# Performance work log

Measured on AMD Instinct MI355X. Metric: run time of the kernel, lower is better.

The kernel has to match this reference:

```python
import jax, jax.numpy as jnp
import numpy as np

EPS = 1e-5

def layer_norm(x, g, b):
    m = jnp.mean(x, axis=-1, keepdims=True)
    v = jnp.var(x, axis=-1, keepdims=True)
    return (x - m) * jax.lax.rsqrt(v + EPS) * g + b

def setup_inputs() -> dict:
    key = jax.random.key(0)
    ks = jax.random.split(key, 10)
    A, T, c_s, c_z, c_atom, c_pair = 1024, 256, 384, 128, 128, 16
    tok = jax.random.randint(ks[0], (A,), 0, T)
    a2t = jax.nn.one_hot(tok, T, dtype=jnp.float32)  # [A, T] one-hot atom->token map
    return {
        "atom_to_token_index": a2t,
        "cl": jax.random.normal(ks[1], (A, c_atom), jnp.float32),
        "plm": jax.random.normal(ks[2], (A, A, c_pair), jnp.float32),
        "ql": jax.random.normal(ks[3], (A, c_atom), jnp.float32),
        "s_trunk": jax.random.normal(ks[4], (T, c_s), jnp.float32),
        "zij": jax.random.normal(ks[5], (T, T, c_z), jnp.float32),
        "rl": jax.random.normal(ks[6], (A, 3), jnp.float32),
        "ln_s_g": jnp.ones((c_s,), jnp.float32),
        "ln_s_b": jnp.zeros((c_s,), jnp.float32),
        "W_s": jax.random.normal(ks[7], (c_s, c_atom), jnp.float32) / np.sqrt(c_s),
        "ln_z_g": jnp.ones((c_z,), jnp.float32),
        "ln_z_b": jnp.zeros((c_z,), jnp.float32),
        "W_z": jax.random.normal(ks[8], (c_z, c_pair), jnp.float32) / np.sqrt(c_z),
        "W_r": jax.random.normal(ks[9], (3, c_atom), jnp.float32) / np.sqrt(3.0),
    }

def reference(atom_to_token_index, cl, plm, ql, s_trunk, zij, rl,
              ln_s_g, ln_s_b, W_s, ln_z_g, ln_z_b, W_z, W_r):
    a2t = atom_to_token_index  # [A, T]
    # token -> atom gather of single rep: sum_t a2t[a,t] * s_trunk[t,:]  -> [A, c_s]
    s_atom = jnp.einsum('at,tc->ac', a2t, s_trunk)
    cl = cl + layer_norm(s_atom, ln_s_g, ln_s_b) @ W_s  # [A, c_atom]
    # token-pair -> atom-pair gather: sum_{t,u} a2t[a,t] a2t[b,u] zij[t,u,:]
    # factored into two one-hot contractions (same math as the dense one-hot outer product)
    z_half = jnp.einsum('at,tuz->auz', a2t, zij)      # [A, T, c_z]
    z_atom = jnp.einsum('auz,bu->abz', z_half, a2t)    # [A, A, c_z]
    plm = plm + layer_norm(z_atom, ln_z_g, ln_z_b) @ W_z  # [A, A, c_pair]
    ql = ql + rl @ W_r  # [A, c_atom]
    return (cl, plm, ql)
```

## Files before the change

kernel.cpp:

```cpp
#include <hip/hip_runtime.h>

#define A_N 1024
#define T_N 256
#define CS 384
#define CZ 128
#define CA 128
#define CP 16
#define LN_EPS 1e-5f

#define ZROWS 64
#define ZPAD 132

__global__ __launch_bounds__(128) void atom_kernel(
        const float* __restrict__ a2t,
        const float* __restrict__ cl,
        const float* __restrict__ ql,
        const float* __restrict__ s_trunk,
        const float* __restrict__ rl,
        const float* __restrict__ g,
        const float* __restrict__ b,
        const float* __restrict__ W_s,
        const float* __restrict__ W_r,
        int* __restrict__ tok,
        float* __restrict__ out_cl,
        float* __restrict__ out_ql) {
    int a = blockIdx.x, tid = threadIdx.x;
    __shared__ int ta_sh;
    __shared__ float xs[CS];
    __shared__ float2 wred[2];

    float v0 = a2t[a * T_N + tid];
    float v1 = a2t[a * T_N + 128 + tid];
    if (v0 > 0.5f) ta_sh = tid;
    if (v1 > 0.5f) ta_sh = 128 + tid;
    __syncthreads();
    int ta = ta_sh;
    if (tid == 0) tok[a] = ta;

    float sum = 0.f, sq = 0.f;
    #pragma unroll
    for (int j = 0; j < 3; ++j) {
        float v = s_trunk[ta * CS + j * 128 + tid];
        xs[j * 128 + tid] = v;
        sum += v; sq += v * v;
    }
    #pragma unroll
    for (int off = 32; off > 0; off >>= 1) {
        sum += __shfl_down(sum, off);
        sq  += __shfl_down(sq,  off);
    }
    if ((tid & 63) == 0) wred[tid >> 6] = make_float2(sum, sq);
    __syncthreads();
    float s  = wred[0].x + wred[1].x;
    float ss = wred[0].y + wred[1].y;
    float m = s * (1.f / CS);
    float rstd = rsqrtf(ss * (1.f / CS) - m * m + LN_EPS);

    float acc = 0.f;
    for (int k = 0; k < CS; ++k) {
        float zn = (xs[k] - m) * rstd * g[k] + b[k];
        acc = fmaf(zn, W_s[k * CA + tid], acc);
    }
    out_cl[a * CA + tid] = cl[a * CA + tid] + acc;

    float r0 = rl[a * 3 + 0], r1 = rl[a * 3 + 1], r2 = rl[a * 3 + 2];
    out_ql[a * CA + tid] = ql[a * CA + tid]
                         + r0 * W_r[tid] + r1 * W_r[CA + tid] + r2 * W_r[2 * CA + tid];
}

__global__ __launch_bounds__(256) void z_kernel(
        const float* __restrict__ zij,
        const float* __restrict__ g,
        const float* __restrict__ b,
        const float* __restrict__ W_z,
        float* __restrict__ Yz) {
    __shared__ float xs[ZROWS * ZPAD];
    __shared__ float wgt[CP * ZPAD];
    __shared__ float2 parts[ZROWS][4];
    __shared__ float msh[ZROWS], rsh[ZROWS];
    __shared__ float2 gb_part[16][16];
    __shared__ float Gw_sh[CP], Bw_sh[CP];

    int t = threadIdx.x;
    size_t base = (size_t)blockIdx.x * ZROWS * CZ;

    const float4* zv = (const float4*)(zij + base);
    #pragma unroll
    for (int n = 0; n < 8; ++n) {
        int idx = n * 256 + t;
        int r = idx >> 5, c = idx & 31;
        *(float4*)&xs[r * ZPAD + c * 4] = zv[idx];
    }
    {
        int j = t & 15, seg = t >> 4;
        float sg = 0.f, sb = 0.f;
        #pragma unroll
        for (int i = 0; i < 8; ++i) {
            int k = seg * 8 + i;
            float w = W_z[k * CP + j];
            float gw = g[k] * w;
            wgt[j * ZPAD + k] = gw;
            sg += gw;
            sb = fmaf(b[k], w, sb);
        }
        gb_part[seg][j] = make_float2(sg, sb);
    }
    __syncthreads();
    if (t < CP) {
        float sg = 0.f, sb = 0.f;
        #pragma unroll
        for (int s = 0; s < 16; ++s) { float2 p = gb_part[s][t]; sg += p.x; sb += p.y; }
        Gw_sh[t] = sg; Bw_sh[t] = sb;
    }
    {
        int r = t >> 2, q = t & 3;
        const float* row = &xs[r * ZPAD + q * 32];
        float s = 0.f, ss = 0.f;
        #pragma unroll
        for (int i = 0; i < 8; ++i) {
            float4 v = *(const float4*)&row[i * 4];
            s += v.x + v.y + v.z + v.w;
            ss += v.x * v.x + v.y * v.y + v.z * v.z + v.w * v.w;
        }
        parts[r][q] = make_float2(s, ss);
    }
    __syncthreads();
    if (t < ZROWS) {
        float s = 0.f, ss = 0.f;
        #pragma unroll
        for (int q = 0; q < 4; ++q) { float2 p = parts[t][q]; s += p.x; ss += p.y; }
        float m = s * (1.f / CZ);
        msh[t] = m;
        rsh[t] = rsqrtf(ss * (1.f / CZ) - m * m + LN_EPS);
    }
    __syncthreads();

    int j = t & 15, rg = t >> 4;
    float acc[4] = {0.f, 0.f, 0.f, 0.f};
    const float* wrow = &wgt[j * ZPAD];
    #pragma unroll 4
    for (int k4 = 0; k4 < 32; ++k4) {
        float4 w = *(const float4*)&wrow[k4 * 4];
        #pragma unroll
        for (int rr = 0; rr < 4; ++rr) {
            float4 x = *(const float4*)&xs[(rg * 4 + rr) * ZPAD + k4 * 4];
            acc[rr] = fmaf(x.x, w.x, acc[rr]);
            acc[rr] = fmaf(x.y, w.y, acc[rr]);
            acc[rr] = fmaf(x.z, w.z, acc[rr]);
            acc[rr] = fmaf(x.w, w.w, acc[rr]);
        }
    }
    float gwj = Gw_sh[j], bwj = Bw_sh[j];
    #pragma unroll
    for (int rr = 0; rr < 4; ++rr) {
        int r = rg * 4 + rr;
        float y = rsh[r] * (acc[rr] - msh[r] * gwj) + bwj;
        size_t grow = (size_t)blockIdx.x * ZROWS + r;
        Yz[grow * CP + j] = y;
    }
}

__global__ __launch_bounds__(256) void plm_kernel(
        const float* __restrict__ plm,
        const float* __restrict__ Yz,
        const int* __restrict__ tok,
        float* __restrict__ out) {
    int tid = threadIdx.x;
    size_t i = (size_t)blockIdx.x * 256 + tid;
    int ta = tok[blockIdx.x >> 4];
    int bb = ((blockIdx.x & 15) << 6) + (tid >> 2);
    int tb = tok[bb];
    float4 pv = ((const float4*)plm)[i];
    float4 yv = ((const float4*)(Yz + (size_t)(ta * T_N + tb) * CP))[tid & 3];
    float4 o;
    o.x = pv.x + yv.x; o.y = pv.y + yv.y;
    o.z = pv.z + yv.z; o.w = pv.w + yv.w;
    ((float4*)out)[i] = o;
}

extern "C" void kernel_launch(void* const* d_in, const int* in_sizes, int n_in,
                              void* d_out, int out_size, void* d_ws, size_t ws_size,
                              hipStream_t stream) {
    const float* a2t     = (const float*)d_in[0];
    const float* cl      = (const float*)d_in[1];
    const float* plm     = (const float*)d_in[2];
    const float* ql      = (const float*)d_in[3];
    const float* s_trunk = (const float*)d_in[4];
    const float* zij     = (const float*)d_in[5];
    const float* rl      = (const float*)d_in[6];
    const float* ln_s_g  = (const float*)d_in[7];
    const float* ln_s_b  = (const float*)d_in[8];
    const float* W_s     = (const float*)d_in[9];
    const float* ln_z_g  = (const float*)d_in[10];
    const float* ln_z_b  = (const float*)d_in[11];
    const float* W_z     = (const float*)d_in[12];
    const float* W_r     = (const float*)d_in[13];

    int*   tok = (int*)d_ws;
    float* Yz  = (float*)((char*)d_ws + 4096);

    float* out_cl  = (float*)d_out;
    float* out_plm = out_cl + A_N * CA;
    float* out_ql  = out_plm + (size_t)A_N * A_N * CP;

    atom_kernel<<<A_N, 128, 0, stream>>>(a2t, cl, ql, s_trunk, rl,
                                         ln_s_g, ln_s_b, W_s, W_r,
                                         tok, out_cl, out_ql);
    z_kernel<<<(T_N * T_N) / ZROWS, 256, 0, stream>>>(zij, ln_z_g, ln_z_b, W_z, Yz);
    plm_kernel<<<((size_t)A_N * A_N * CP / 4) / 256, 256, 0, stream>>>(plm, Yz, tok, out_plm);
}
```

Measured before the change: 200.9 us.

## Use bf16 MFMA for z projection and compute s projection per token

Measured after the change: 191.9 us. 4.5% less time.

```diff
diff --git a/kernel.cpp b/kernel.cpp
--- a/kernel.cpp
+++ b/kernel.cpp
@@ -8,39 +8,22 @@
 #define CP 16
 #define LN_EPS 1e-5f
 
-#define ZROWS 64
-#define ZPAD 132
-
-__global__ __launch_bounds__(128) void atom_kernel(
-        const float* __restrict__ a2t,
-        const float* __restrict__ cl,
-        const float* __restrict__ ql,
+typedef __bf16  bf16x8 __attribute__((ext_vector_type(8)));
+typedef float   f32x4  __attribute__((ext_vector_type(4)));
+
+__global__ __launch_bounds__(128) void s_kernel(
         const float* __restrict__ s_trunk,
-        const float* __restrict__ rl,
         const float* __restrict__ g,
         const float* __restrict__ b,
         const float* __restrict__ W_s,
-        const float* __restrict__ W_r,
-        int* __restrict__ tok,
-        float* __restrict__ out_cl,
-        float* __restrict__ out_ql) {
-    int a = blockIdx.x, tid = threadIdx.x;
-    __shared__ int ta_sh;
+        float* __restrict__ Ys) {
+    int t = blockIdx.x, tid = threadIdx.x;
     __shared__ float xs[CS];
     __shared__ float2 wred[2];
-
-    float v0 = a2t[a * T_N + tid];
-    float v1 = a2t[a * T_N + 128 + tid];
-    if (v0 > 0.5f) ta_sh = tid;
-    if (v1 > 0.5f) ta_sh = 128 + tid;
-    __syncthreads();
-    int ta = ta_sh;
-    if (tid == 0) tok[a] = ta;
-
     float sum = 0.f, sq = 0.f;
     #pragma unroll
     for (int j = 0; j < 3; ++j) {
-        float v = s_trunk[ta * CS + j * 128 + tid];
+        float v = s_trunk[t * CS + j * 128 + tid];
         xs[j * 128 + tid] = v;
         sum += v; sq += v * v;
     }
@@ -56,41 +39,34 @@
     float m = s * (1.f / CS);
     float rstd = rsqrtf(ss * (1.f / CS) - m * m + LN_EPS);
 
-    float acc = 0.f;
-    for (int k = 0; k < CS; ++k) {
-        float zn = (xs[k] - m) * rstd * g[k] + b[k];
-        acc = fmaf(zn, W_s[k * CA + tid], acc);
-    }
-    out_cl[a * CA + tid] = cl[a * CA + tid] + acc;
-
-    float r0 = rl[a * 3 + 0], r1 = rl[a * 3 + 1], r2 = rl[a * 3 + 2];
-    out_ql[a * CA + tid] = ql[a * CA + tid]
-                         + r0 * W_r[tid] + r1 * W_r[CA + tid] + r2 * W_r[2 * CA + tid];
-}
-
-__global__ __launch_bounds__(256) void z_kernel(
+    float a0 = 0.f, a1 = 0.f, a2 = 0.f, a3 = 0.f;
+    for (int k = 0; k < CS; k += 4) {
+        float z0 = (xs[k + 0] - m) * rstd * g[k + 0] + b[k + 0];
+        float z1 = (xs[k + 1] - m) * rstd * g[k + 1] + b[k + 1];
+        float z2 = (xs[k + 2] - m) * rstd * g[k + 2] + b[k + 2];
+        float z3 = (xs[k + 3] - m) * rstd * g[k + 3] + b[k + 3];
+        a0 = fmaf(z0, W_s[(k + 0) * CA + tid], a0);
+        a1 = fmaf(z1, W_s[(k + 1) * CA + tid], a1);
+        a2 = fmaf(z2, W_s[(k + 2) * CA + tid], a2);
+        a3 = fmaf(z3, W_s[(k + 3) * CA + tid], a3);
+    }
+    Ys[t * CA + tid] = (a0 + a1) + (a2 + a3);
+}
+
+#define WSTRIDE 136
+
+__global__ __launch_bounds__(256) void z_mfma_kernel(
         const float* __restrict__ zij,
         const float* __restrict__ g,
         const float* __restrict__ b,
         const float* __restrict__ W_z,
         float* __restrict__ Yz) {
-    __shared__ float xs[ZROWS * ZPAD];
-    __shared__ float wgt[CP * ZPAD];
-    __shared__ float2 parts[ZROWS][4];
-    __shared__ float msh[ZROWS], rsh[ZROWS];
+    __shared__ __bf16 wb[CP * WSTRIDE];
     __shared__ float2 gb_part[16][16];
     __shared__ float Gw_sh[CP], Bw_sh[CP];
 
     int t = threadIdx.x;
-    size_t base = (size_t)blockIdx.x * ZROWS * CZ;
-
-    const float4* zv = (const float4*)(zij + base);
-    #pragma unroll
-    for (int n = 0; n < 8; ++n) {
-        int idx = n * 256 + t;
-        int r = idx >> 5, c = idx & 31;
-        *(float4*)&xs[r * ZPAD + c * 4] = zv[idx];
-    }
+
     {
         int j = t & 15, seg = t >> 4;
         float sg = 0.f, sb = 0.f;
@@ -99,7 +75,7 @@
             int k = seg * 8 + i;
             float w = W_z[k * CP + j];
             float gw = g[k] * w;
-            wgt[j * ZPAD + k] = gw;
+            wb[j * WSTRIDE + k] = (__bf16)gw;
             sg += gw;
             sb = fmaf(b[k], w, sb);
         }
@@ -112,52 +88,83 @@
         for (int s = 0; s < 16; ++s) { float2 p = gb_part[s][t]; sg += p.x; sb += p.y; }
         Gw_sh[t] = sg; Bw_sh[t] = sb;
     }
-    {
-        int r = t >> 2, q = t & 3;
-        const float* row = &xs[r * ZPAD + q * 32];
-        float s = 0.f, ss = 0.f;
-        #pragma unroll
-        for (int i = 0; i < 8; ++i) {
-            float4 v = *(const float4*)&row[i * 4];
-            s += v.x + v.y + v.z + v.w;
-            ss += v.x * v.x + v.y * v.y + v.z * v.z + v.w * v.w;
-        }
-        parts[r][q] = make_float2(s, ss);
-    }
-    __syncthreads();
-    if (t < ZROWS) {
-        float s = 0.f, ss = 0.f;
-        #pragma unroll
-        for (int q = 0; q < 4; ++q) { float2 p = parts[t][q]; s += p.x; ss += p.y; }
-        float m = s * (1.f / CZ);
-        msh[t] = m;
-        rsh[t] = rsqrtf(ss * (1.f / CZ) - m * m + LN_EPS);
-    }
-    __syncthreads();
-
-    int j = t & 15, rg = t >> 4;
-    float acc[4] = {0.f, 0.f, 0.f, 0.f};
-    const float* wrow = &wgt[j * ZPAD];
-    #pragma unroll 4
-    for (int k4 = 0; k4 < 32; ++k4) {
-        float4 w = *(const float4*)&wrow[k4 * 4];
-        #pragma unroll
-        for (int rr = 0; rr < 4; ++rr) {
-            float4 x = *(const float4*)&xs[(rg * 4 + rr) * ZPAD + k4 * 4];
-            acc[rr] = fmaf(x.x, w.x, acc[rr]);
-            acc[rr] = fmaf(x.y, w.y, acc[rr]);
-            acc[rr] = fmaf(x.z, w.z, acc[rr]);
-            acc[rr] = fmaf(x.w, w.w, acc[rr]);
-        }
-    }
-    float gwj = Gw_sh[j], bwj = Bw_sh[j];
-    #pragma unroll
-    for (int rr = 0; rr < 4; ++rr) {
-        int r = rg * 4 + rr;
-        float y = rsh[r] * (acc[rr] - msh[r] * gwj) + bwj;
-        size_t grow = (size_t)blockIdx.x * ZROWS + r;
-        Yz[grow * CP + j] = y;
-    }
+
+    int wave = t >> 6, lane = t & 63;
+    int m    = lane & 15, quad = lane >> 4;
+    size_t grow = (size_t)blockIdx.x * 64 + wave * 16 + m;
+
+    const float4* zrow = (const float4*)(zij + grow * CZ);
+    float4 xv[8];
+    #pragma unroll
+    for (int s = 0; s < 4; ++s) {
+        xv[2 * s]     = zrow[quad * 2 + 8 * s];
+        xv[2 * s + 1] = zrow[quad * 2 + 8 * s + 1];
+    }
+
+    float sum = 0.f, sq = 0.f;
+    #pragma unroll
+    for (int i = 0; i < 8; ++i) {
+        float4 v = xv[i];
+        sum += (v.x + v.y) + (v.z + v.w);
+        sq  += v.x * v.x + v.y * v.y + v.z * v.z + v.w * v.w;
+    }
+    sum += __shfl_xor(sum, 16);  sq += __shfl_xor(sq, 16);
+    sum += __shfl_xor(sum, 32);  sq += __shfl_xor(sq, 32);
+    float mval = sum * (1.f / CZ);
+    float rstd = rsqrtf(sq * (1.f / CZ) - mval * mval + LN_EPS);
+
+    __syncthreads();
+
+    f32x4 acc = {0.f, 0.f, 0.f, 0.f};
+    #pragma unroll
+    for (int s = 0; s < 4; ++s) {
+        float4 v0 = xv[2 * s], v1 = xv[2 * s + 1];
+        bf16x8 af;
+        af[0] = (__bf16)v0.x; af[1] = (__bf16)v0.y;
+        af[2] = (__bf16)v0.z; af[3] = (__bf16)v0.w;
+        af[4] = (__bf16)v1.x; af[5] = (__bf16)v1.y;
+        af[6] = (__bf16)v1.z; af[7] = (__bf16)v1.w;
+        bf16x8 bf = *(const bf16x8*)&wb[m * WSTRIDE + quad * 8 + 32 * s];
+        acc = __builtin_amdgcn_mfma_f32_16x16x32_bf16(af, bf, acc, 0, 0, 0);
+    }
+
+    float gwj = Gw_sh[m], bwj = Bw_sh[m];
+    size_t obase = (size_t)blockIdx.x * 64 + wave * 16;
+    #pragma unroll
+    for (int i = 0; i < 4; ++i) {
+        int r = quad * 4 + i;
+        float mi = __shfl(mval, r);
+        float ri = __shfl(rstd, r);
+        float y = ri * (acc[i] - mi * gwj) + bwj;
+        Yz[(obase + r) * CP + m] = y;
+    }
+}
+
+__global__ __launch_bounds__(128) void atom_kernel(
+        const float* __restrict__ a2t,
+        const float* __restrict__ cl,
+        const float* __restrict__ ql,
+        const float* __restrict__ rl,
+        const float* __restrict__ Ys,
+        const float* __restrict__ W_r,
+        int* __restrict__ tok,
+        float* __restrict__ out_cl,
+        float* __restrict__ out_ql) {
+    int a = blockIdx.x, tid = threadIdx.x;
+    __shared__ int ta_sh;
+    float v0 = a2t[a * T_N + tid];
+    float v1 = a2t[a * T_N + 128 + tid];
+    if (v0 > 0.5f) ta_sh = tid;
+    if (v1 > 0.5f) ta_sh = 128 + tid;
+    __syncthreads();
+    int ta = ta_sh;
+    if (tid == 0) tok[a] = ta;
+
+    out_cl[a * CA + tid] = cl[a * CA + tid] + Ys[ta * CA + tid];
+
+    float r0 = rl[a * 3 + 0], r1 = rl[a * 3 + 1], r2 = rl[a * 3 + 2];
+    out_ql[a * CA + tid] = ql[a * CA + tid]
+                         + r0 * W_r[tid] + r1 * W_r[CA + tid] + r2 * W_r[2 * CA + tid];
 }
 
 __global__ __launch_bounds__(256) void plm_kernel(
@@ -197,15 +204,15 @@
     const float* W_r     = (const float*)d_in[13];
 
     int*   tok = (int*)d_ws;
-    float* Yz  = (float*)((char*)d_ws + 4096);
+    float* Ys  = (float*)((char*)d_ws + 4096);
+    float* Yz  = (float*)((char*)d_ws + 4096 + 131072);
 
     float* out_cl  = (float*)d_out;
     float* out_plm = out_cl + A_N * CA;
     float* out_ql  = out_plm + (size_t)A_N * A_N * CP;
 
-    atom_kernel<<<A_N, 128, 0, stream>>>(a2t, cl, ql, s_trunk, rl,
-                                         ln_s_g, ln_s_b, W_s, W_r,
-                                         tok, out_cl, out_ql);
-    z_kernel<<<(T_N * T_N) / ZROWS, 256, 0, stream>>>(zij, ln_z_g, ln_z_b, W_z, Yz);
+    s_kernel<<<T_N, 128, 0, stream>>>(s_trunk, ln_s_g, ln_s_b, W_s, Ys);
+    z_mfma_kernel<<<(T_N * T_N) / 64, 256, 0, stream>>>(zij, ln_z_g, ln_z_b, W_z, Yz);
+    atom_kernel<<<A_N, 128, 0, stream>>>(a2t, cl, ql, rl, Ys, W_r, tok, out_cl, out_ql);
     plm_kernel<<<((size_t)A_N * A_N * CP / 4) / 256, 256, 0, stream>>>(plm, Yz, tok, out_plm);
 }
```
